# Kernel optimization log

Hardware: AMD Instinct MI355X
Metric: run time of the kernel (lower is better)

Reference implementation:

```python
import jax, jax.numpy as jnp
import numpy as np

TOPK_FRAC = 0.05  # init arg `topk` (fraction of pool kept)


def setup_inputs() -> dict:
    key = jax.random.key(0)
    k1, k2 = jax.random.split(key)
    x = jax.random.normal(k1, (16, 256, 32, 32), dtype=jnp.float32)
    # nn.Parameter(torch.rand(P, C)) -> uniform [0, 1)
    visual_concept_pool = jax.random.uniform(k2, (2048, 256), dtype=jnp.float32)
    return {"x": x, "visual_concept_pool": visual_concept_pool}


def reference(x, visual_concept_pool):
    n, c, h, w = x.shape
    P = visual_concept_pool.shape[0]
    L = h * w
    xf = x.reshape(n, c, L)                              # [n, c, L]
    # dot_product[n, P, L] = pool @ xf
    dot = jnp.einsum('pc,ncl->npl', visual_concept_pool, xf)
    pool_norm = jnp.sqrt(jnp.sum(visual_concept_pool ** 2, axis=1))   # [P]
    x_norm = jnp.sqrt(jnp.sum(xf ** 2, axis=1))                        # [n, L]
    cos = dot / (pool_norm[None, :, None] * x_norm[:, None, :])       # [n, P, L]

    # mode 1.1: top-k over the pool dimension per (n, pixel)
    keep = int(TOPK_FRAC * P)
    cos_t = jnp.transpose(cos, (0, 2, 1))                # [n, L, P]
    _, idx = jax.lax.top_k(jnp.abs(cos_t), keep)         # [n, L, keep]
    mask = jnp.zeros_like(cos_t).at[
        jnp.arange(n)[:, None, None],
        jnp.arange(L)[None, :, None],
        idx,
    ].set(1.0)                                           # [n, L, P]
    masked = cos_t * mask
    normed = masked / jnp.sum(masked, axis=-1, keepdims=True)  # renormalize over P
    # reconstruct[n, c, L] = pool^T @ cos
    recon = jnp.einsum('pc,nlp->ncl', visual_concept_pool, normed)
    return recon.reshape(n, c, h, w)
```

## Files before the change

### kernel.cpp

```cpp
#include <hip/hip_runtime.h>
#include <hip/hip_fp16.h>

typedef unsigned short u16;
typedef _Float16 half8 __attribute__((ext_vector_type(8)));
typedef float floatx4 __attribute__((ext_vector_type(4)));

#define C_DIM 256
#define P_DIM 2048
#define L_DIM 1024
#define N_DIM 16
#define KEEP 102
#define KPAD 104
#define QTR_PIX 4096
#define SCALE 256.0f

__device__ __forceinline__ void st8(u16* dst, const u16* s) {
  uint4 u;
  u.x = (unsigned)s[0] | ((unsigned)s[1] << 16);
  u.y = (unsigned)s[2] | ((unsigned)s[3] << 16);
  u.z = (unsigned)s[4] | ((unsigned)s[5] << 16);
  u.w = (unsigned)s[6] | ((unsigned)s[7] << 16);
  *(uint4*)dst = u;
}

__device__ __forceinline__ u16 f2h_ftz(float v) {
  if (fabsf(v) < 6.103515625e-5f) return 0;
  return __half_as_ushort(__float2half(v));
}

__device__ __forceinline__ void gl_lds16(const u16* g, u16* l) {
  __builtin_amdgcn_global_load_lds(
      (const __attribute__((address_space(1))) unsigned int*)g,
      (__attribute__((address_space(3))) unsigned int*)l, 16, 0, 0);
}

union SMem {
  u16 sB[2][2][8][512];
  struct { float tbuf[8][260]; int2 kpw[8][KPAD]; } sel;
};

__global__ __launch_bounds__(256) void k_pinv(const float* __restrict__ pool,
                                              float* __restrict__ pinv) {
  int p = blockIdx.x * 256 + threadIdx.x;
  const float4* row = (const float4*)(pool + (size_t)p * C_DIM);
  float s = 0.f;
#pragma unroll
  for (int i = 0; i < C_DIM / 4; ++i) {
    float4 v = row[i];
    s += v.x * v.x + v.y * v.y + v.z * v.z + v.w * v.w;
  }
  pinv[p] = 1.0f / sqrtf(s);
}

__device__ __forceinline__ void packpool_body(int b,
                                              const float* __restrict__ pool,
                                              const float* __restrict__ pinv,
                                              u16* __restrict__ ah,
                                              u16* __restrict__ al,
                                              u16* __restrict__ ph) {
  int tid = b * 512 + threadIdx.x;
  int lane = tid & 63;
  int ks = (tid >> 6) & 7;
  int pm = tid >> 9;
  int p = pm * 16 + (lane & 15);
  int c0 = ks * 32 + ((lane >> 4) << 3);
  float sc = pinv[p] * SCALE;
  const float* src = pool + (size_t)p * C_DIM + c0;
  u16 h8[8], l8[8], p8[8];
#pragma unroll
  for (int j = 0; j < 8; ++j) {
    float raw = src[j];
    p8[j] = __half_as_ushort(__float2half(raw));
    float v = raw * sc;
    u16 h = f2h_ftz(v);
    float r = v - __half2float(__ushort_as_half(h));
    h8[j] = h;
    l8[j] = f2h_ftz(r);
  }
  size_t o = (size_t)tid * 8;
  st8(ah + o, h8); st8(al + o, l8);
  st8(ph + (size_t)p * C_DIM + c0, p8);
}

__device__ __forceinline__ void packx_body(int pb, int pq,
                                           const float* __restrict__ x,
                                           u16* __restrict__ xh,
                                           u16* __restrict__ xl) {
  int t = threadIdx.x;
  int lane = t & 63;
  int ks = (t >> 6) & 7;
  int pn = pq * 256 + pb;
  int pix = pn * 16 + (lane & 15);
  int n = pix >> 10, l = pix & 1023;
  int c0 = ks * 32 + ((lane >> 4) << 3);
  const float* src = x + ((size_t)(n * C_DIM + c0)) * L_DIM + l;
  u16 h8[8], l8[8];
#pragma unroll
  for (int j = 0; j < 8; ++j) {
    float v = src[(size_t)j * L_DIM] * SCALE;
    u16 h = f2h_ftz(v);
    float r = v - __half2float(__ushort_as_half(h));
    h8[j] = h;
    l8[j] = f2h_ftz(r);
  }
  size_t o = ((size_t)pn * 512 + (size_t)ks * 64 + lane) * 8;
  st8(xh + o, h8); st8(xl + o, l8);
}

__global__ __launch_bounds__(512) void k_pre(const float* __restrict__ pool,
                                             const float* __restrict__ pinv,
                                             u16* __restrict__ ah,
                                             u16* __restrict__ al,
                                             u16* __restrict__ ph,
                                             const float* __restrict__ x,
                                             u16* __restrict__ xh,
                                             u16* __restrict__ xl) {
  int b = blockIdx.x;
  if (b < 128) packpool_body(b, pool, pinv, ah, al, ph);
  else packx_body(b - 128, 0, x, xh, xl);
}

__device__ __forceinline__ void mfma_body(int b, int mq,
                                          const u16* __restrict__ ah_,
                                          const u16* __restrict__ al_,
                                          const u16* __restrict__ xh_,
                                          const u16* __restrict__ xl_,
                                          float* __restrict__ sbuf,
                                          u16 (*sB)[2][8][512]) {
  const int t = threadIdx.x, lane = t & 63, w = t >> 6;
  const int pT = b & 15, pixT = b >> 4;
  const int pm = pT * 8 + w;
  const int pnBase = mq * 256 + pixT * 8;
  const half8* A8h = (const half8*)ah_;
  const half8* A8l = (const half8*)al_;
  const u16* xsrc[2] = {xh_, xl_};

  floatx4 acc[8];
#pragma unroll
  for (int nt = 0; nt < 8; ++nt) acc[nt] = (floatx4){0.f, 0.f, 0.f, 0.f};

#pragma unroll
  for (int q = 0; q < 2; ++q) {
    int id = w * 2 + q;
    int arr = id >> 3, nt = id & 7;
    gl_lds16(xsrc[arr] + ((size_t)(pnBase + nt) * 512 + lane) * 8,
             &sB[0][arr][nt][0]);
  }
  __syncthreads();

#pragma unroll 1
  for (int ks = 0; ks < 8; ++ks) {
    const int cur = ks & 1;
    half8 aH, aL;
    {
      size_t idx = (size_t)pm * 512 + (size_t)ks * 64 + lane;
      aH = A8h[idx]; aL = A8l[idx];
    }
    if (ks < 7) {
#pragma unroll
      for (int q = 0; q < 2; ++q) {
        int id = w * 2 + q;
        int arr = id >> 3, nt = id & 7;
        gl_lds16(xsrc[arr] + ((size_t)(pnBase + nt) * 512 + (ks + 1) * 64 + lane) * 8,
                 &sB[cur ^ 1][arr][nt][0]);
      }
    }
#pragma unroll
    for (int nt = 0; nt < 8; ++nt) {
      half8 bh = *(const half8*)&sB[cur][0][nt][lane * 8];
      half8 bl = *(const half8*)&sB[cur][1][nt][lane * 8];
      floatx4 c = acc[nt];
      c = __builtin_amdgcn_mfma_f32_16x16x32_f16(aH, bh, c, 0, 0, 0);
      c = __builtin_amdgcn_mfma_f32_16x16x32_f16(aH, bl, c, 0, 0, 0);
      c = __builtin_amdgcn_mfma_f32_16x16x32_f16(aL, bh, c, 0, 0, 0);
      acc[nt] = c;
    }
    __syncthreads();
  }

  const int qr = lane >> 4, cl = lane & 15;
  const int pix0 = pixT * 128;
  const int pcol = pT * 128 + w * 16;
#pragma unroll
  for (int nt = 0; nt < 8; ++nt) {
    float* dst = sbuf + (size_t)(pix0 + nt * 16 + cl) * P_DIM + pcol + qr * 4;
    *(float4*)dst = make_float4(acc[nt][0], acc[nt][1], acc[nt][2], acc[nt][3]);
  }
}

__device__ __forceinline__ void select_body(int b, int sq,
                                            const float* __restrict__ sbuf,
                                            const u16* __restrict__ pool_h,
                                            float* __restrict__ out,
                                            float (*tbuf)[260],
                                            int2 (*kpw)[KPAD]) {
  const int t = threadIdx.x;
  const int lane = t & 63;
  const int wv = t >> 6;
  const int gp0 = sq * QTR_PIX + b * 8;
  const int n = gp0 >> 10;
  const int l0 = gp0 & 1023;
  const float* sp = sbuf + (size_t)(b * 8 + wv) * P_DIM;

  float4 v[8];
#pragma unroll
  for (int q = 0; q < 8; ++q) v[q] = *(const float4*)(sp + q * 256 + lane * 4);

  if (lane < KPAD - KEEP) kpw[wv][KEEP + lane] = make_int2(0, 0);

  float M = 0.f;
#pragma unroll
  for (int q = 0; q < 8; ++q) {
    M = fmaxf(M, fabsf(v[q].x)); M = fmaxf(M, fabsf(v[q].y));
    M = fmaxf(M, fabsf(v[q].z)); M = fmaxf(M, fabsf(v[q].w));
  }
#pragma unroll
  for (int off = 1; off < 64; off <<= 1) M = fmaxf(M, __shfl_xor(M, off));
  const unsigned bitsM = __float_as_uint(M);

  auto countGE = [&](float mf) -> unsigned {
    unsigned cnt = 0;
#pragma unroll
    for (int q = 0; q < 8; ++q) {
      cnt += (unsigned)__popcll(__ballot(fabsf(v[q].x) >= mf));
      cnt += (unsigned)__popcll(__ballot(fabsf(v[q].y) >= mf));
      cnt += (unsigned)__popcll(__ballot(fabsf(v[q].z) >= mf));
      cnt += (unsigned)__popcll(__ballot(fabsf(v[q].w) >= mf));
    }
    return cnt;
  };

  const unsigned t1 = (bitsM > (1u << 23)) ? bitsM - (1u << 23) : 1u;
  const unsigned t2 = (bitsM > (2u << 23)) ? bitsM - (2u << 23) : 1u;
  const unsigned t3 = (bitsM > (3u << 23)) ? bitsM - (3u << 23) : 1u;
  const unsigned t4 = (bitsM > (5u << 23)) ? bitsM - (5u << 23) : 1u;
  const float g1 = __uint_as_float(t1), g2 = __uint_as_float(t2);
  const float g3 = __uint_as_float(t3), g4 = __uint_as_float(t4);
  unsigned c1 = 0, c2 = 0, c3 = 0, c4 = 0;
#pragma unroll
  for (int q = 0; q < 8; ++q) {
    const float* f = (const float*)&v[q];
#pragma unroll
    for (int rr = 0; rr < 4; ++rr) {
      float av = fabsf(f[rr]);
      c1 += (unsigned)__popcll(__ballot(av >= g1));
      c2 += (unsigned)__popcll(__ballot(av >= g2));
      c3 += (unsigned)__popcll(__ballot(av >= g3));
      c4 += (unsigned)__popcll(__ballot(av >= g4));
    }
  }

  unsigned lo = 0u, hi = 1u, cl_ = P_DIM, ch_ = 0u;
  bool exact = false;
  if (c1 == (unsigned)KEEP)      { lo = t1; exact = true; }
  else if (c2 == (unsigned)KEEP) { lo = t2; exact = true; }
  else if (c3 == (unsigned)KEEP) { lo = t3; exact = true; }
  else if (c4 == (unsigned)KEEP) { lo = t4; exact = true; }
  else if (c1 > (unsigned)KEEP)  { lo = t1; cl_ = c1; hi = bitsM + 1u; ch_ = 0u; }
  else if (c2 > (unsigned)KEEP)  { lo = t2; cl_ = c2; hi = t1; ch_ = c1; }
  else if (c3 > (unsigned)KEEP)  { lo = t3; cl_ = c3; hi = t2; ch_ = c2; }
  else if (c4 > (unsigned)KEEP)  { lo = t4; cl_ = c4; hi = t3; ch_ = c3; }
  else                           { lo = 0u; cl_ = P_DIM; hi = t4; ch_ = c4; }

  int it = 0;
  while (!exact && hi - lo > 1u) {
    unsigned span = hi - lo;
    unsigned step;
    if ((it++ & 1) == 0) {
      step = (unsigned)((float)span * (float)(cl_ - KEEP) / (float)(cl_ - ch_));
    } else {
      step = span >> 1;
    }
    if (step < 1u) step = 1u;
    else if (step > span - 1u) step = span - 1u;
    unsigned m = lo + step;
    unsigned cnt = countGE(__uint_as_float(m));
    if (cnt == (unsigned)KEEP) { lo = m; exact = true; break; }
    if (cnt > (unsigned)KEEP) { lo = m; cl_ = cnt; } else { hi = m; ch_ = cnt; }
  }
  const float V = __uint_as_float(lo);
  const float Vp = exact ? V : __uint_as_float(lo + 1u);

  unsigned rrem = 0u;
  if (!exact) {
    unsigned gt = countGE(Vp);
    rrem = (unsigned)KEEP - gt;
  }

  unsigned gmask[8], tmask[8];
#pragma unroll
  for (int q = 0; q < 8; ++q) {
    const float* f = (const float*)&v[q];
    unsigned gm = 0, tm = 0;
#pragma unroll
    for (int rr = 0; rr < 4; ++rr) {
      float av = fabsf(f[rr]);
      if (av >= Vp) gm |= (1u << rr);
      else if (av >= V) tm |= (1u << rr);
    }
    gmask[q] = gm; tmask[q] = tm;
  }

  const unsigned long long lowm = (1ull << lane) - 1ull;
  unsigned base = 0, tiebase = 0;
  float Ssum = 0.f;
#pragma unroll
  for (int q = 0; q < 8; ++q) {
    const float* f = (const float*)&v[q];
    unsigned km = gmask[q];
    if (rrem != 0u) {
      unsigned teq = 0, myeqb = 0;
#pragma unroll
      for (int rr = 0; rr < 4; ++rr) {
        unsigned long long beq = __ballot((tmask[q] >> rr) & 1u);
        teq += (unsigned)__popcll(beq);
        myeqb += (unsigned)__popcll(beq & lowm);
      }
      unsigned cum = 0;
#pragma unroll
      for (int rr = 0; rr < 4; ++rr) {
        if ((tmask[q] >> rr) & 1u) {
          if (tiebase + myeqb + cum < rrem) km |= (1u << rr);
          ++cum;
        }
      }
      tiebase += teq;
    }
    unsigned long long bk[4];
    unsigned tot = 0, myb = 0;
#pragma unroll
    for (int rr = 0; rr < 4; ++rr) {
      bk[rr] = __ballot((km >> rr) & 1u);
      tot += (unsigned)__popcll(bk[rr]);
      myb += (unsigned)__popcll(bk[rr] & lowm);
    }
    {
      unsigned cum = 0;
#pragma unroll
      for (int rr = 0; rr < 4; ++rr) {
        if ((km >> rr) & 1u) {
          unsigned pos = base + myb + cum;
          kpw[wv][pos] = make_int2((q * 256 + lane * 4 + rr) << 9,
                                   __float_as_int(f[rr]));
          Ssum += f[rr];
          ++cum;
        }
      }
    }
    base += tot;
  }

#pragma unroll
  for (int off = 1; off < 64; off <<= 1) Ssum += __shfl_xor(Ssum, off);
  const float invS = 1.0f / Ssum;

  __builtin_amdgcn_wave_barrier();

  float a0 = 0.f, a1 = 0.f, a2 = 0.f, a3 = 0.f;
  const char* pb = (const char*)(pool_h + 4 * lane);
  int2 eA[4], eB[4];
  uint2 rA[4], rB[4];

  auto PROC = [&](const int2* e, const uint2* r) {
#pragma unroll
    for (int j = 0; j < 4; ++j) {
      float w2 = __int_as_float(e[j].y);
      unsigned rx = r[j].x, ry = r[j].y;
      asm volatile("v_fma_mix_f32 %0, %1, %2, %0 op_sel:[0,0,0] op_sel_hi:[0,1,0]"
                   : "+v"(a0) : "v"(w2), "v"(rx));
      asm volatile("v_fma_mix_f32 %0, %1, %2, %0 op_sel:[0,1,0] op_sel_hi:[0,1,0]"
                   : "+v"(a1) : "v"(w2), "v"(rx));
      asm volatile("v_fma_mix_f32 %0, %1, %2, %0 op_sel:[0,0,0] op_sel_hi:[0,1,0]"
                   : "+v"(a2) : "v"(w2), "v"(ry));
      asm volatile("v_fma_mix_f32 %0, %1, %2, %0 op_sel:[0,1,0] op_sel_hi:[0,1,0]"
                   : "+v"(a3) : "v"(w2), "v"(ry));
    }
  };

#pragma unroll
  for (int j = 0; j < 4; ++j) eA[j] = kpw[wv][j];
#pragma unroll
  for (int j = 0; j < 4; ++j)
    rA[j] = *(const uint2*)(pb + (unsigned)eA[j].x);

#pragma unroll 1
  for (int k = 0; k < KPAD; k += 8) {
    const int kb = k + 4;
#pragma unroll
    for (int j = 0; j < 4; ++j) eB[j] = kpw[wv][kb + j];
#pragma unroll
    for (int j = 0; j < 4; ++j)
      rB[j] = *(const uint2*)(pb + (unsigned)eB[j].x);
    PROC(eA, rA);
    const int ka = (k + 8 < KPAD) ? k + 8 : 0;
#pragma unroll
    for (int j = 0; j < 4; ++j) eA[j] = kpw[wv][ka + j];
#pragma unroll
    for (int j = 0; j < 4; ++j)
      rA[j] = *(const uint2*)(pb + (unsigned)eA[j].x);
    PROC(eB, rB);
  }
  a0 *= invS; a1 *= invS; a2 *= invS; a3 *= invS;

  *(float4*)&tbuf[wv][4 * lane] = make_float4(a0, a1, a2, a3);
  __syncthreads();

  {
    int c = t >> 1, lq = t & 1;
    float4 o = make_float4(tbuf[4 * lq + 0][c], tbuf[4 * lq + 1][c],
                           tbuf[4 * lq + 2][c], tbuf[4 * lq + 3][c]);
    *(float4*)(out + ((size_t)(n * C_DIM + c)) * L_DIM + l0 + 4 * lq) = o;
  }
}

__global__ __launch_bounds__(512, 4) void k_main(const u16* __restrict__ ah_,
                                                 const u16* __restrict__ al_,
                                                 const u16* __restrict__ xh_,
                                                 const u16* __restrict__ xl_,
                                                 const u16* __restrict__ ph,
                                                 const float* __restrict__ x,
                                                 float* __restrict__ sbuf0,
                                                 float* __restrict__ sbuf1,
                                                 float* __restrict__ out,
                                                 int mq, int sq, int pq) {
  __shared__ __align__(16) SMem sm;
  const int b = blockIdx.x;
  const int nsel = (sq >= 0) ? 512 : 0;
  const int npk = (pq >= 0) ? 256 : 0;
  if (b < nsel) {
    select_body(b, sq, (sq & 1) ? sbuf1 : sbuf0, ph, out, sm.sel.tbuf, sm.sel.kpw);
  } else if (b < nsel + npk) {
    packx_body(b - nsel, pq, x, (u16*)xh_, (u16*)xl_);
  } else {
    mfma_body(b - nsel - npk, mq, ah_, al_, xh_, xl_, (mq & 1) ? sbuf1 : sbuf0, sm.sB);
  }
}

extern "C" void kernel_launch(void* const* d_in, const int* in_sizes, int n_in,
                              void* d_out, int out_size, void* d_ws, size_t ws_size,
                              hipStream_t stream) {
  const float* x = (const float*)d_in[0];
  const float* pool = (const float*)d_in[1];
  float* out = (float*)d_out;
  char* wsb = (char*)d_ws;
  float* sbuf0 = (float*)wsb;
  float* sbuf1 = (float*)(wsb + 33554432);
  u16* xh = (u16*)(wsb + 67108864);
  u16* xl = xh + 4194304;
  u16* ah = xl + 4194304;
  u16* al = ah + 524288;
  u16* ph = al + 524288;
  float* pinv = (float*)(ph + 524288);

  k_pinv<<<P_DIM / 256, 256, 0, stream>>>(pool, pinv);
  k_pre<<<384, 512, 0, stream>>>(pool, pinv, ah, al, ph, x, xh, xl);

  k_main<<<768, 512, 0, stream>>>(ah, al, xh, xl, ph, x, sbuf0, sbuf1, out, 0, -1, 1);
  k_main<<<1280, 512, 0, stream>>>(ah, al, xh, xl, ph, x, sbuf0, sbuf1, out, 1, 0, 2);
  k_main<<<1280, 512, 0, stream>>>(ah, al, xh, xl, ph, x, sbuf0, sbuf1, out, 2, 1, 3);
  k_main<<<1024, 512, 0, stream>>>(ah, al, xh, xl, ph, x, sbuf0, sbuf1, out, 3, 2, -1);
  k_main<<<512, 512, 0, stream>>>(ah, al, xh, xl, ph, x, sbuf0, sbuf1, out, -1, 3, -1);
}
```

Baseline: 249.1 us.

## Widen select-phase pool gathers to 16 bytes with half-wave split, reorder block roles

The reconstruction gather now reads 16-byte rows per lane covering 8 channels, with the two half-waves each processing alternate selected entries, and the partial sums are combined through a cross-half shuffle. The packed int2 offset/weight array is split into separate offset and weight arrays in LDS. Block dispatch order also changes so MFMA blocks come before packx blocks. The intent is fewer, wider global loads per selected entry; the cost is an extra shuffle reduction and half the lanes idle during the store.

```diff
diff --git a/kernel.cpp b/kernel.cpp
--- a/kernel.cpp
+++ b/kernel.cpp
@@ -36,7 +36,11 @@
 
 union SMem {
   u16 sB[2][2][8][512];
-  struct { float tbuf[8][260]; int2 kpw[8][KPAD]; } sel;
+  struct {
+    float tbuf[8][260];
+    int   kpo[8][KPAD];
+    float kw[8][KPAD];
+  } sel;
 };
 
 __global__ __launch_bounds__(256) void k_pinv(const float* __restrict__ pool,
@@ -193,7 +197,8 @@
                                             const u16* __restrict__ pool_h,
                                             float* __restrict__ out,
                                             float (*tbuf)[260],
-                                            int2 (*kpw)[KPAD]) {
+                                            int (*kpo)[KPAD],
+                                            float (*kw)[KPAD]) {
   const int t = threadIdx.x;
   const int lane = t & 63;
   const int wv = t >> 6;
@@ -206,7 +211,7 @@
 #pragma unroll
   for (int q = 0; q < 8; ++q) v[q] = *(const float4*)(sp + q * 256 + lane * 4);
 
-  if (lane < KPAD - KEEP) kpw[wv][KEEP + lane] = make_int2(0, 0);
+  if (lane < KPAD - KEEP) { kpo[wv][KEEP + lane] = 0; kw[wv][KEEP + lane] = 0.f; }
 
   float M = 0.f;
 #pragma unroll
@@ -340,8 +345,8 @@
       for (int rr = 0; rr < 4; ++rr) {
         if ((km >> rr) & 1u) {
           unsigned pos = base + myb + cum;
-          kpw[wv][pos] = make_int2((q * 256 + lane * 4 + rr) << 9,
-                                   __float_as_int(f[rr]));
+          kpo[wv][pos] = (q * 256 + lane * 4 + rr) << 9;
+          kw[wv][pos] = f[rr];
           Ssum += f[rr];
           ++cum;
         }
@@ -357,15 +362,24 @@
   __builtin_amdgcn_wave_barrier();
 
   float a0 = 0.f, a1 = 0.f, a2 = 0.f, a3 = 0.f;
-  const char* pb = (const char*)(pool_h + 4 * lane);
-  int2 eA[4], eB[4];
-  uint2 rA[4], rB[4];
-
-  auto PROC = [&](const int2* e, const uint2* r) {
+  float a4 = 0.f, a5 = 0.f, a6 = 0.f, a7 = 0.f;
+  const int half = lane >> 5;
+  const char* pbase = (const char*)pool_h + (lane & 31) * 16;
+
+  int oA[4], oB[4];
+  uint4 rA[4], rB[4];
+
+  auto LOADG = [&](int g, int* o, uint4* r) {
+#pragma unroll
+    for (int j = 0; j < 4; ++j) o[j] = kpo[wv][8 * g + 2 * j + half];
+#pragma unroll
+    for (int j = 0; j < 4; ++j) r[j] = *(const uint4*)(pbase + (unsigned)o[j]);
+  };
+  auto PROC = [&](int g, const uint4* r) {
 #pragma unroll
     for (int j = 0; j < 4; ++j) {
-      float w2 = __int_as_float(e[j].y);
-      unsigned rx = r[j].x, ry = r[j].y;
+      float w2 = kw[wv][8 * g + 2 * j + half];
+      unsigned rx = r[j].x, ry = r[j].y, rz = r[j].z, rw = r[j].w;
       asm volatile("v_fma_mix_f32 %0, %1, %2, %0 op_sel:[0,0,0] op_sel_hi:[0,1,0]"
                    : "+v"(a0) : "v"(w2), "v"(rx));
       asm volatile("v_fma_mix_f32 %0, %1, %2, %0 op_sel:[0,1,0] op_sel_hi:[0,1,0]"
@@ -374,35 +388,37 @@
                    : "+v"(a2) : "v"(w2), "v"(ry));
       asm volatile("v_fma_mix_f32 %0, %1, %2, %0 op_sel:[0,1,0] op_sel_hi:[0,1,0]"
                    : "+v"(a3) : "v"(w2), "v"(ry));
+      asm volatile("v_fma_mix_f32 %0, %1, %2, %0 op_sel:[0,0,0] op_sel_hi:[0,1,0]"
+                   : "+v"(a4) : "v"(w2), "v"(rz));
+      asm volatile("v_fma_mix_f32 %0, %1, %2, %0 op_sel:[0,1,0] op_sel_hi:[0,1,0]"
+                   : "+v"(a5) : "v"(w2), "v"(rz));
+      asm volatile("v_fma_mix_f32 %0, %1, %2, %0 op_sel:[0,0,0] op_sel_hi:[0,1,0]"
+                   : "+v"(a6) : "v"(w2), "v"(rw));
+      asm volatile("v_fma_mix_f32 %0, %1, %2, %0 op_sel:[0,1,0] op_sel_hi:[0,1,0]"
+                   : "+v"(a7) : "v"(w2), "v"(rw));
     }
   };
 
-#pragma unroll
-  for (int j = 0; j < 4; ++j) eA[j] = kpw[wv][j];
-#pragma unroll
-  for (int j = 0; j < 4; ++j)
-    rA[j] = *(const uint2*)(pb + (unsigned)eA[j].x);
-
+  LOADG(0, oA, rA);
 #pragma unroll 1
-  for (int k = 0; k < KPAD; k += 8) {
-    const int kb = k + 4;
-#pragma unroll
-    for (int j = 0; j < 4; ++j) eB[j] = kpw[wv][kb + j];
-#pragma unroll
-    for (int j = 0; j < 4; ++j)
-      rB[j] = *(const uint2*)(pb + (unsigned)eB[j].x);
-    PROC(eA, rA);
-    const int ka = (k + 8 < KPAD) ? k + 8 : 0;
-#pragma unroll
-    for (int j = 0; j < 4; ++j) eA[j] = kpw[wv][ka + j];
-#pragma unroll
-    for (int j = 0; j < 4; ++j)
-      rA[j] = *(const uint2*)(pb + (unsigned)eA[j].x);
-    PROC(eB, rB);
-  }
-  a0 *= invS; a1 *= invS; a2 *= invS; a3 *= invS;
-
-  *(float4*)&tbuf[wv][4 * lane] = make_float4(a0, a1, a2, a3);
+  for (int g = 0; g < 12; g += 2) {
+    LOADG(g + 1, oB, rB);
+    PROC(g, rA);
+    LOADG(g + 2, oA, rA);
+    PROC(g + 1, rB);
+  }
+  PROC(12, rA);
+
+  a0 += __shfl_xor(a0, 32); a1 += __shfl_xor(a1, 32);
+  a2 += __shfl_xor(a2, 32); a3 += __shfl_xor(a3, 32);
+  a4 += __shfl_xor(a4, 32); a5 += __shfl_xor(a5, 32);
+  a6 += __shfl_xor(a6, 32); a7 += __shfl_xor(a7, 32);
+
+  if (lane < 32) {
+    int ch0 = lane * 8;
+    *(float4*)&tbuf[wv][ch0] = make_float4(a0 * invS, a1 * invS, a2 * invS, a3 * invS);
+    *(float4*)&tbuf[wv][ch0 + 4] = make_float4(a4 * invS, a5 * invS, a6 * invS, a7 * invS);
+  }
   __syncthreads();
 
   {
@@ -426,13 +442,14 @@
   __shared__ __align__(16) SMem sm;
   const int b = blockIdx.x;
   const int nsel = (sq >= 0) ? 512 : 0;
-  const int npk = (pq >= 0) ? 256 : 0;
+  const int nmf = (mq >= 0) ? 512 : 0;
   if (b < nsel) {
-    select_body(b, sq, (sq & 1) ? sbuf1 : sbuf0, ph, out, sm.sel.tbuf, sm.sel.kpw);
-  } else if (b < nsel + npk) {
-    packx_body(b - nsel, pq, x, (u16*)xh_, (u16*)xl_);
+    select_body(b, sq, (sq & 1) ? sbuf1 : sbuf0, ph, out,
+                sm.sel.tbuf, sm.sel.kpo, sm.sel.kw);
+  } else if (b < nsel + nmf) {
+    mfma_body(b - nsel, mq, ah_, al_, xh_, xl_, (mq & 1) ? sbuf1 : sbuf0, sm.sB);
   } else {
-    mfma_body(b - nsel - npk, mq, ah_, al_, xh_, xl_, (mq & 1) ? sbuf1 : sbuf0, sm.sB);
+    packx_body(b - nsel - nmf, pq, x, (u16*)xh_, (u16*)xl_);
   }
 }
 
```

After: 248.3 us. No clear change (-0.3%).

## Rebalance pipelined stages with uneven chunk sizes and a smaller-block final select

Applied to the files above, without the earlier changes.

Replaces the four equal quarter-sized stages with uneven chunks: small first and last chunks and larger middle ones, so the pipeline fills and drains faster. The mfma, select and pack work per launch is now given by explicit offsets and block counts. A new k_selT kernel with 4 waves per block handles the final select chunk, giving more blocks for the tail. This aims to cut pipeline fill and drain bubbles but adds two more launches and a more complex buffer ping-pong schedule.

```diff
diff --git a/kernel.cpp b/kernel.cpp
--- a/kernel.cpp
+++ b/kernel.cpp
@@ -11,7 +11,6 @@
 #define N_DIM 16
 #define KEEP 102
 #define KPAD 104
-#define QTR_PIX 4096
 #define SCALE 256.0f
 
 __device__ __forceinline__ void st8(u16* dst, const u16* s) {
@@ -36,7 +35,10 @@
 
 union SMem {
   u16 sB[2][2][8][512];
-  struct { float tbuf[8][260]; int2 kpw[8][KPAD]; } sel;
+  struct {
+    float tbuf[8][260];
+    int2  kpw[8][KPAD];
+  } sel;
 };
 
 __global__ __launch_bounds__(256) void k_pinv(const float* __restrict__ pool,
@@ -82,14 +84,14 @@
   st8(ph + (size_t)p * C_DIM + c0, p8);
 }
 
-__device__ __forceinline__ void packx_body(int pb, int pq,
+__device__ __forceinline__ void packx_body(int pb, int pn0,
                                            const float* __restrict__ x,
                                            u16* __restrict__ xh,
                                            u16* __restrict__ xl) {
   int t = threadIdx.x;
   int lane = t & 63;
   int ks = (t >> 6) & 7;
-  int pn = pq * 256 + pb;
+  int pn = pn0 + pb;
   int pix = pn * 16 + (lane & 15);
   int n = pix >> 10, l = pix & 1023;
   int c0 = ks * 32 + ((lane >> 4) << 3);
@@ -120,7 +122,7 @@
   else packx_body(b - 128, 0, x, xh, xl);
 }
 
-__device__ __forceinline__ void mfma_body(int b, int mq,
+__device__ __forceinline__ void mfma_body(int b, int pn0,
                                           const u16* __restrict__ ah_,
                                           const u16* __restrict__ al_,
                                           const u16* __restrict__ xh_,
@@ -130,7 +132,7 @@
   const int t = threadIdx.x, lane = t & 63, w = t >> 6;
   const int pT = b & 15, pixT = b >> 4;
   const int pm = pT * 8 + w;
-  const int pnBase = mq * 256 + pixT * 8;
+  const int pnBase = pn0 + pixT * 8;
   const half8* A8h = (const half8*)ah_;
   const half8* A8l = (const half8*)al_;
   const u16* xsrc[2] = {xh_, xl_};
@@ -188,7 +190,8 @@
   }
 }
 
-__device__ __forceinline__ void select_body(int b, int sq,
+template <int NW>
+__device__ __forceinline__ void select_body(int b, int gp0base,
                                             const float* __restrict__ sbuf,
                                             const u16* __restrict__ pool_h,
                                             float* __restrict__ out,
@@ -197,10 +200,10 @@
   const int t = threadIdx.x;
   const int lane = t & 63;
   const int wv = t >> 6;
-  const int gp0 = sq * QTR_PIX + b * 8;
+  const int gp0 = gp0base + b * NW;
   const int n = gp0 >> 10;
   const int l0 = gp0 & 1023;
-  const float* sp = sbuf + (size_t)(b * 8 + wv) * P_DIM;
+  const float* sp = sbuf + (size_t)(b * NW + wv) * P_DIM;
 
   float4 v[8];
 #pragma unroll
@@ -380,24 +383,20 @@
 #pragma unroll
   for (int j = 0; j < 4; ++j) eA[j] = kpw[wv][j];
 #pragma unroll
-  for (int j = 0; j < 4; ++j)
-    rA[j] = *(const uint2*)(pb + (unsigned)eA[j].x);
-
+  for (int j = 0; j < 4; ++j) rA[j] = *(const uint2*)(pb + (unsigned)eA[j].x);
 #pragma unroll 1
   for (int k = 0; k < KPAD; k += 8) {
     const int kb = k + 4;
 #pragma unroll
     for (int j = 0; j < 4; ++j) eB[j] = kpw[wv][kb + j];
 #pragma unroll
-    for (int j = 0; j < 4; ++j)
-      rB[j] = *(const uint2*)(pb + (unsigned)eB[j].x);
+    for (int j = 0; j < 4; ++j) rB[j] = *(const uint2*)(pb + (unsigned)eB[j].x);
     PROC(eA, rA);
     const int ka = (k + 8 < KPAD) ? k + 8 : 0;
 #pragma unroll
     for (int j = 0; j < 4; ++j) eA[j] = kpw[wv][ka + j];
 #pragma unroll
-    for (int j = 0; j < 4; ++j)
-      rA[j] = *(const uint2*)(pb + (unsigned)eA[j].x);
+    for (int j = 0; j < 4; ++j) rA[j] = *(const uint2*)(pb + (unsigned)eA[j].x);
     PROC(eB, rB);
   }
   a0 *= invS; a1 *= invS; a2 *= invS; a3 *= invS;
@@ -405,11 +404,15 @@
   *(float4*)&tbuf[wv][4 * lane] = make_float4(a0, a1, a2, a3);
   __syncthreads();
 
-  {
+  if (NW == 8) {
     int c = t >> 1, lq = t & 1;
     float4 o = make_float4(tbuf[4 * lq + 0][c], tbuf[4 * lq + 1][c],
                            tbuf[4 * lq + 2][c], tbuf[4 * lq + 3][c]);
     *(float4*)(out + ((size_t)(n * C_DIM + c)) * L_DIM + l0 + 4 * lq) = o;
+  } else {
+    int c = t;
+    float4 o = make_float4(tbuf[0][c], tbuf[1][c], tbuf[2][c], tbuf[3][c]);
+    *(float4*)(out + ((size_t)(n * C_DIM + c)) * L_DIM + l0) = o;
   }
 }
 
@@ -419,21 +422,30 @@
                                                  const u16* __restrict__ xl_,
                                                  const u16* __restrict__ ph,
                                                  const float* __restrict__ x,
-                                                 float* __restrict__ sbuf0,
-                                                 float* __restrict__ sbuf1,
+                                                 float* __restrict__ msbuf,
+                                                 const float* __restrict__ ssbuf,
                                                  float* __restrict__ out,
-                                                 int mq, int sq, int pq) {
+                                                 int m_pn0, int m_nblk,
+                                                 int s_gp0, int s_nblk,
+                                                 int p_pn0, int p_nblk) {
   __shared__ __align__(16) SMem sm;
   const int b = blockIdx.x;
-  const int nsel = (sq >= 0) ? 512 : 0;
-  const int npk = (pq >= 0) ? 256 : 0;
-  if (b < nsel) {
-    select_body(b, sq, (sq & 1) ? sbuf1 : sbuf0, ph, out, sm.sel.tbuf, sm.sel.kpw);
-  } else if (b < nsel + npk) {
-    packx_body(b - nsel, pq, x, (u16*)xh_, (u16*)xl_);
+  if (b < s_nblk) {
+    select_body<8>(b, s_gp0, ssbuf, ph, out, sm.sel.tbuf, sm.sel.kpw);
+  } else if (b < s_nblk + p_nblk) {
+    packx_body(b - s_nblk, p_pn0, x, (u16*)xh_, (u16*)xl_);
   } else {
-    mfma_body(b - nsel - npk, mq, ah_, al_, xh_, xl_, (mq & 1) ? sbuf1 : sbuf0, sm.sB);
-  }
+    mfma_body(b - s_nblk - p_nblk, m_pn0, ah_, al_, xh_, xl_, msbuf, sm.sB);
+  }
+}
+
+__global__ __launch_bounds__(256, 8) void k_selT(const float* __restrict__ sbuf,
+                                                 const u16* __restrict__ ph,
+                                                 float* __restrict__ out,
+                                                 int gp0base) {
+  __shared__ __align__(16) float tbuf[4][260];
+  __shared__ int2 kpw[4][KPAD];
+  select_body<4>(blockIdx.x, gp0base, sbuf, ph, out, tbuf, kpw);
 }
 
 extern "C" void kernel_launch(void* const* d_in, const int* in_sizes, int n_in,
@@ -443,8 +455,8 @@
   const float* pool = (const float*)d_in[1];
   float* out = (float*)d_out;
   char* wsb = (char*)d_ws;
-  float* sbuf0 = (float*)wsb;
-  float* sbuf1 = (float*)(wsb + 33554432);
+  float* sb0 = (float*)wsb;
+  float* sb1 = (float*)(wsb + 33554432);
   u16* xh = (u16*)(wsb + 67108864);
   u16* xl = xh + 4194304;
   u16* ah = xl + 4194304;
@@ -453,11 +465,19 @@
   float* pinv = (float*)(ph + 524288);
 
   k_pinv<<<P_DIM / 256, 256, 0, stream>>>(pool, pinv);
-  k_pre<<<384, 512, 0, stream>>>(pool, pinv, ah, al, ph, x, xh, xl);
-
-  k_main<<<768, 512, 0, stream>>>(ah, al, xh, xl, ph, x, sbuf0, sbuf1, out, 0, -1, 1);
-  k_main<<<1280, 512, 0, stream>>>(ah, al, xh, xl, ph, x, sbuf0, sbuf1, out, 1, 0, 2);
-  k_main<<<1280, 512, 0, stream>>>(ah, al, xh, xl, ph, x, sbuf0, sbuf1, out, 2, 1, 3);
-  k_main<<<1024, 512, 0, stream>>>(ah, al, xh, xl, ph, x, sbuf0, sbuf1, out, 3, 2, -1);
-  k_main<<<512, 512, 0, stream>>>(ah, al, xh, xl, ph, x, sbuf0, sbuf1, out, -1, 3, -1);
-}
+  k_pre<<<256, 512, 0, stream>>>(pool, pinv, ah, al, ph, x, xh, xl);
+
+  k_main<<<384, 512, 0, stream>>>(ah, al, xh, xl, ph, x, sb0, sb0, out,
+                                  0, 256, 0, 0, 128, 128);
+  k_main<<<768, 512, 0, stream>>>(ah, al, xh, xl, ph, x, sb1, sb0, out,
+                                  128, 256, 0, 256, 256, 256);
+  k_main<<<1024, 512, 0, stream>>>(ah, al, xh, xl, ph, x, sb0, sb1, out,
+                                   256, 512, 2048, 256, 512, 256);
+  k_main<<<1152, 512, 0, stream>>>(ah, al, xh, xl, ph, x, sb1, sb0, out,
+                                   512, 512, 4096, 512, 768, 128);
+  k_main<<<896, 512, 0, stream>>>(ah, al, xh, xl, ph, x, sb0, sb1, out,
+                                  768, 256, 8192, 512, 896, 128);
+  k_main<<<512, 512, 0, stream>>>(ah, al, xh, xl, ph, x, sb1, sb0, out,
+                                  896, 256, 12288, 256, 0, 0);
+  k_selT<<<512, 256, 0, stream>>>(sb1, ph, out, 14336);
+}
```

After: 271.1 us. 1.09x slower.

## Replace sparse top-k gather reconstruction with dense fp16 MFMA over masked weights

Applied to the files above, without the earlier changes.

The reconstruction step no longer compacts the 102 selected pool indices and gathers pool rows with scalar fma_mix. Each block instead writes a dense, zero-filled fp16 weight row of all 2048 pool entries per pixel into swizzled LDS. It then runs a 16x16x32 MFMA against a pool copy pre-transposed into MFMA fragment layout. This trades about 20x more arithmetic (dense over P) for matrix-core throughput, regular loads and no index compaction. It also adds fp16 rounding of the normalized weights and uncoalesced scalar output stores, with only 8 of 16 MFMA columns used.

```diff
diff --git a/kernel.cpp b/kernel.cpp
--- a/kernel.cpp
+++ b/kernel.cpp
@@ -10,7 +10,6 @@
 #define L_DIM 1024
 #define N_DIM 16
 #define KEEP 102
-#define KPAD 104
 #define QTR_PIX 4096
 #define SCALE 256.0f
 
@@ -36,7 +35,7 @@
 
 union SMem {
   u16 sB[2][2][8][512];
-  struct { float tbuf[8][260]; int2 kpw[8][KPAD]; } sel;
+  u16 z[8][2048];
 };
 
 __global__ __launch_bounds__(256) void k_pinv(const float* __restrict__ pool,
@@ -57,7 +56,7 @@
                                               const float* __restrict__ pinv,
                                               u16* __restrict__ ah,
                                               u16* __restrict__ al,
-                                              u16* __restrict__ ph) {
+                                              u16* __restrict__ phT) {
   int tid = b * 512 + threadIdx.x;
   int lane = tid & 63;
   int ks = (tid >> 6) & 7;
@@ -79,7 +78,15 @@
   }
   size_t o = (size_t)tid * 8;
   st8(ah + o, h8); st8(al + o, l8);
-  st8(ph + (size_t)p * C_DIM + c0, p8);
+  {
+    int ksr = p >> 5, lhr = (p >> 3) & 3, jr = p & 7;
+#pragma unroll
+    for (int i = 0; i < 8; ++i) {
+      int c = c0 + i;
+      size_t idx = ((size_t)((c >> 4) * 64 + ksr) * 64 + ((c & 15) + 16 * lhr)) * 8 + jr;
+      phT[idx] = p8[i];
+    }
+  }
 }
 
 __device__ __forceinline__ void packx_body(int pb, int pq,
@@ -111,12 +118,12 @@
                                              const float* __restrict__ pinv,
                                              u16* __restrict__ ah,
                                              u16* __restrict__ al,
-                                             u16* __restrict__ ph,
+                                             u16* __restrict__ phT,
                                              const float* __restrict__ x,
                                              u16* __restrict__ xh,
                                              u16* __restrict__ xl) {
   int b = blockIdx.x;
-  if (b < 128) packpool_body(b, pool, pinv, ah, al, ph);
+  if (b < 128) packpool_body(b, pool, pinv, ah, al, phT);
   else packx_body(b - 128, 0, x, xh, xl);
 }
 
@@ -188,25 +195,20 @@
   }
 }
 
-__device__ __forceinline__ void select_body(int b, int sq,
-                                            const float* __restrict__ sbuf,
-                                            const u16* __restrict__ pool_h,
-                                            float* __restrict__ out,
-                                            float (*tbuf)[260],
-                                            int2 (*kpw)[KPAD]) {
+__device__ __forceinline__ void selr_body(int b, int sq,
+                                          const float* __restrict__ sbuf,
+                                          const u16* __restrict__ phT,
+                                          float* __restrict__ out,
+                                          u16 (*z)[2048]) {
   const int t = threadIdx.x;
   const int lane = t & 63;
   const int wv = t >> 6;
   const int gp0 = sq * QTR_PIX + b * 8;
-  const int n = gp0 >> 10;
-  const int l0 = gp0 & 1023;
   const float* sp = sbuf + (size_t)(b * 8 + wv) * P_DIM;
 
   float4 v[8];
 #pragma unroll
   for (int q = 0; q < 8; ++q) v[q] = *(const float4*)(sp + q * 256 + lane * 4);
-
-  if (lane < KPAD - KEEP) kpw[wv][KEEP + lane] = make_int2(0, 0);
 
   float M = 0.f;
 #pragma unroll
@@ -287,129 +289,105 @@
     rrem = (unsigned)KEEP - gt;
   }
 
-  unsigned gmask[8], tmask[8];
+  unsigned km[8];
 #pragma unroll
   for (int q = 0; q < 8; ++q) {
     const float* f = (const float*)&v[q];
-    unsigned gm = 0, tm = 0;
-#pragma unroll
-    for (int rr = 0; rr < 4; ++rr) {
-      float av = fabsf(f[rr]);
-      if (av >= Vp) gm |= (1u << rr);
-      else if (av >= V) tm |= (1u << rr);
-    }
-    gmask[q] = gm; tmask[q] = tm;
-  }
-
-  const unsigned long long lowm = (1ull << lane) - 1ull;
-  unsigned base = 0, tiebase = 0;
-  float Ssum = 0.f;
-#pragma unroll
-  for (int q = 0; q < 8; ++q) {
-    const float* f = (const float*)&v[q];
-    unsigned km = gmask[q];
-    if (rrem != 0u) {
+    unsigned gm = 0;
+#pragma unroll
+    for (int rr = 0; rr < 4; ++rr)
+      if (fabsf(f[rr]) >= Vp) gm |= (1u << rr);
+    km[q] = gm;
+  }
+  if (rrem != 0u) {
+    const unsigned long long lowm = (1ull << lane) - 1ull;
+    unsigned tiebase = 0;
+#pragma unroll
+    for (int q = 0; q < 8; ++q) {
+      const float* f = (const float*)&v[q];
+      unsigned tm = 0;
+#pragma unroll
+      for (int rr = 0; rr < 4; ++rr) {
+        float av = fabsf(f[rr]);
+        if (av >= V && av < Vp) tm |= (1u << rr);
+      }
       unsigned teq = 0, myeqb = 0;
 #pragma unroll
       for (int rr = 0; rr < 4; ++rr) {
-        unsigned long long beq = __ballot((tmask[q] >> rr) & 1u);
+        unsigned long long beq = __ballot((tm >> rr) & 1u);
         teq += (unsigned)__popcll(beq);
         myeqb += (unsigned)__popcll(beq & lowm);
       }
       unsigned cum = 0;
 #pragma unroll
       for (int rr = 0; rr < 4; ++rr) {
-        if ((tmask[q] >> rr) & 1u) {
-          if (tiebase + myeqb + cum < rrem) km |= (1u << rr);
+        if ((tm >> rr) & 1u) {
+          if (tiebase + myeqb + cum < rrem) km[q] |= (1u << rr);
           ++cum;
         }
       }
       tiebase += teq;
     }
-    unsigned long long bk[4];
-    unsigned tot = 0, myb = 0;
-#pragma unroll
-    for (int rr = 0; rr < 4; ++rr) {
-      bk[rr] = __ballot((km >> rr) & 1u);
-      tot += (unsigned)__popcll(bk[rr]);
-      myb += (unsigned)__popcll(bk[rr] & lowm);
-    }
-    {
-      unsigned cum = 0;
-#pragma unroll
-      for (int rr = 0; rr < 4; ++rr) {
-        if ((km >> rr) & 1u) {
-          unsigned pos = base + myb + cum;
-          kpw[wv][pos] = make_int2((q * 256 + lane * 4 + rr) << 9,
-                                   __float_as_int(f[rr]));
-          Ssum += f[rr];
-          ++cum;
-        }
-      }
-    }
-    base += tot;
-  }
-
+  }
+
+  float Ssum = 0.f;
+#pragma unroll
+  for (int q = 0; q < 8; ++q) {
+    const float* f = (const float*)&v[q];
+#pragma unroll
+    for (int rr = 0; rr < 4; ++rr)
+      if ((km[q] >> rr) & 1u) Ssum += f[rr];
+  }
 #pragma unroll
   for (int off = 1; off < 64; off <<= 1) Ssum += __shfl_xor(Ssum, off);
   const float invS = 1.0f / Ssum;
 
-  __builtin_amdgcn_wave_barrier();
-
-  float a0 = 0.f, a1 = 0.f, a2 = 0.f, a3 = 0.f;
-  const char* pb = (const char*)(pool_h + 4 * lane);
-  int2 eA[4], eB[4];
-  uint2 rA[4], rB[4];
-
-  auto PROC = [&](const int2* e, const uint2* r) {
-#pragma unroll
-    for (int j = 0; j < 4; ++j) {
-      float w2 = __int_as_float(e[j].y);
-      unsigned rx = r[j].x, ry = r[j].y;
-      asm volatile("v_fma_mix_f32 %0, %1, %2, %0 op_sel:[0,0,0] op_sel_hi:[0,1,0]"
-                   : "+v"(a0) : "v"(w2), "v"(rx));
-      asm volatile("v_fma_mix_f32 %0, %1, %2, %0 op_sel:[0,1,0] op_sel_hi:[0,1,0]"
-                   : "+v"(a1) : "v"(w2), "v"(rx));
-      asm volatile("v_fma_mix_f32 %0, %1, %2, %0 op_sel:[0,0,0] op_sel_hi:[0,1,0]"
-                   : "+v"(a2) : "v"(w2), "v"(ry));
-      asm volatile("v_fma_mix_f32 %0, %1, %2, %0 op_sel:[0,1,0] op_sel_hi:[0,1,0]"
-                   : "+v"(a3) : "v"(w2), "v"(ry));
-    }
-  };
-
-#pragma unroll
-  for (int j = 0; j < 4; ++j) eA[j] = kpw[wv][j];
-#pragma unroll
-  for (int j = 0; j < 4; ++j)
-    rA[j] = *(const uint2*)(pb + (unsigned)eA[j].x);
-
-#pragma unroll 1
-  for (int k = 0; k < KPAD; k += 8) {
-    const int kb = k + 4;
-#pragma unroll
-    for (int j = 0; j < 4; ++j) eB[j] = kpw[wv][kb + j];
-#pragma unroll
-    for (int j = 0; j < 4; ++j)
-      rB[j] = *(const uint2*)(pb + (unsigned)eB[j].x);
-    PROC(eA, rA);
-    const int ka = (k + 8 < KPAD) ? k + 8 : 0;
-#pragma unroll
-    for (int j = 0; j < 4; ++j) eA[j] = kpw[wv][ka + j];
-#pragma unroll
-    for (int j = 0; j < 4; ++j)
-      rA[j] = *(const uint2*)(pb + (unsigned)eA[j].x);
-    PROC(eB, rB);
-  }
-  a0 *= invS; a1 *= invS; a2 *= invS; a3 *= invS;
-
-  *(float4*)&tbuf[wv][4 * lane] = make_float4(a0, a1, a2, a3);
+  {
+    char* zr = (char*)&z[wv][0];
+#pragma unroll
+    for (int q = 0; q < 8; ++q) {
+      const float* f = (const float*)&v[q];
+      u16 h4[4];
+#pragma unroll
+      for (int rr = 0; rr < 4; ++rr) {
+        float val = ((km[q] >> rr) & 1u) ? invS * f[rr] : 0.f;
+        h4[rr] = __half_as_ushort(__float2half(val));
+      }
+      unsigned w0 = (unsigned)h4[0] | ((unsigned)h4[1] << 16);
+      unsigned w1 = (unsigned)h4[2] | ((unsigned)h4[3] << 16);
+      *(uint2*)(zr + ((q * 512 + lane * 8) ^ (wv << 4))) = make_uint2(w0, w1);
+    }
+  }
   __syncthreads();
 
-  {
-    int c = t >> 1, lq = t & 1;
-    float4 o = make_float4(tbuf[4 * lq + 0][c], tbuf[4 * lq + 1][c],
-                           tbuf[4 * lq + 2][c], tbuf[4 * lq + 3][c]);
-    *(float4*)(out + ((size_t)(n * C_DIM + c)) * L_DIM + l0 + 4 * lq) = o;
+  const half8* A = (const half8*)phT;
+  const int pm0 = wv * 2;
+  const int zrow = lane & 7;
+  const char* zb = (const char*)&z[zrow][0];
+  const int boff = ((lane >> 4) << 4);
+
+  floatx4 acc0 = (floatx4){0.f, 0.f, 0.f, 0.f};
+  floatx4 acc1 = (floatx4){0.f, 0.f, 0.f, 0.f};
+#pragma unroll 8
+  for (int ks = 0; ks < 64; ++ks) {
+    half8 bz = *(const half8*)(zb + ((ks * 64 + boff) ^ (zrow << 4)));
+    half8 a0 = A[(size_t)(pm0 * 64 + ks) * 64 + lane];
+    half8 a1 = A[(size_t)((pm0 + 1) * 64 + ks) * 64 + lane];
+    acc0 = __builtin_amdgcn_mfma_f32_16x16x32_f16(a0, bz, acc0, 0, 0, 0);
+    acc1 = __builtin_amdgcn_mfma_f32_16x16x32_f16(a1, bz, acc1, 0, 0, 0);
+  }
+
+  const int col = lane & 15;
+  if (col < 8) {
+    int pix = gp0 + col;
+    int n = pix >> 10, l = pix & 1023;
+    int r0 = (lane >> 4) * 4;
+#pragma unroll
+    for (int r = 0; r < 4; ++r) {
+      int c = pm0 * 16 + r0 + r;
+      out[((size_t)(n * C_DIM + c)) * L_DIM + l] = acc0[r];
+      out[((size_t)(n * C_DIM + c + 16)) * L_DIM + l] = acc1[r];
+    }
   }
 }
 
@@ -417,7 +395,7 @@
                                                  const u16* __restrict__ al_,
                                                  const u16* __restrict__ xh_,
                                                  const u16* __restrict__ xl_,
-                                                 const u16* __restrict__ ph,
+                                                 const u16* __restrict__ phT,
                                                  const float* __restrict__ x,
                                                  float* __restrict__ sbuf0,
                                                  float* __restrict__ sbuf1,
@@ -428,7 +406,7 @@
   const int nsel = (sq >= 0) ? 512 : 0;
   const int npk = (pq >= 0) ? 256 : 0;
   if (b < nsel) {
-    select_body(b, sq, (sq & 1) ? sbuf1 : sbuf0, ph, out, sm.sel.tbuf, sm.sel.kpw);
+    selr_body(b, sq, (sq & 1) ? sbuf1 : sbuf0, phT, out, sm.z);
   } else if (b < nsel + npk) {
     packx_body(b - nsel, pq, x, (u16*)xh_, (u16*)xl_);
   } else {
@@ -449,15 +427,15 @@
   u16* xl = xh + 4194304;
   u16* ah = xl + 4194304;
   u16* al = ah + 524288;
-  u16* ph = al + 524288;
-  float* pinv = (float*)(ph + 524288);
+  u16* phT = al + 524288;
+  float* pinv = (float*)(phT + 524288);
 
   k_pinv<<<P_DIM / 256, 256, 0, stream>>>(pool, pinv);
-  k_pre<<<384, 512, 0, stream>>>(pool, pinv, ah, al, ph, x, xh, xl);
-
-  k_main<<<768, 512, 0, stream>>>(ah, al, xh, xl, ph, x, sbuf0, sbuf1, out, 0, -1, 1);
-  k_main<<<1280, 512, 0, stream>>>(ah, al, xh, xl, ph, x, sbuf0, sbuf1, out, 1, 0, 2);
-  k_main<<<1280, 512, 0, stream>>>(ah, al, xh, xl, ph, x, sbuf0, sbuf1, out, 2, 1, 3);
-  k_main<<<1024, 512, 0, stream>>>(ah, al, xh, xl, ph, x, sbuf0, sbuf1, out, 3, 2, -1);
-  k_main<<<512, 512, 0, stream>>>(ah, al, xh, xl, ph, x, sbuf0, sbuf1, out, -1, 3, -1);
-}
+  k_pre<<<384, 512, 0, stream>>>(pool, pinv, ah, al, phT, x, xh, xl);
+
+  k_main<<<768, 512, 0, stream>>>(ah, al, xh, xl, phT, x, sbuf0, sbuf1, out, 0, -1, 1);
+  k_main<<<1280, 512, 0, stream>>>(ah, al, xh, xl, phT, x, sbuf0, sbuf1, out, 1, 0, 2);
+  k_main<<<1280, 512, 0, stream>>>(ah, al, xh, xl, phT, x, sbuf0, sbuf1, out, 2, 1, 3);
+  k_main<<<1024, 512, 0, stream>>>(ah, al, xh, xl, phT, x, sbuf0, sbuf1, out, 3, 2, -1);
+  k_main<<<512, 512, 0, stream>>>(ah, al, xh, xl, phT, x, sbuf0, sbuf1, out, -1, 3, -1);
+}
```

Result: slower. 277.5 us (+11.4%).
